# Optimization experiments

Measured on AMD Instinct MI355X. Metric: run time of the kernel, lower is better.

Reference implementation:

```python
import jax, jax.numpy as jnp
import numpy as np

# Dimensions: B graphs of NPG nodes each (equal sizes -> padding == reshape, exact)
B, NPG, DIN, H, E, DOUT, K_ORDER = 8, 4096, 128, 4, 262144, 128, 4
BETA = 0.5
N = B * NPG


def setup_inputs() -> dict:
    key = jax.random.key(0)
    k = jax.random.split(key, 12)
    s = 1.0 / np.sqrt(DIN)
    so = 1.0 / np.sqrt(H * DIN)
    x = jax.random.normal(k[0], (N, DIN), jnp.float32)
    Wq_w = jax.random.normal(k[1], (H * DIN, DIN), jnp.float32) * s
    Wq_b = jax.random.normal(k[2], (H * DIN,), jnp.float32) * 0.01
    Wk_w = jax.random.normal(k[3], (H * DIN, DIN), jnp.float32) * s
    Wk_b = jax.random.normal(k[4], (H * DIN,), jnp.float32) * 0.01
    Wo_w = jax.random.normal(k[5], (DOUT, H * DIN), jnp.float32) * so
    Wo_b = jax.random.normal(k[6], (DOUT,), jnp.float32) * 0.01
    # edges constrained within graphs (faithful to per-graph data)
    g = jax.random.randint(k[7], (E,), 0, B)
    row = g * NPG + jax.random.randint(k[8], (E,), 0, NPG)
    col = g * NPG + jax.random.randint(k[9], (E,), 0, NPG)
    edge_index = jnp.stack([row, col]).astype(jnp.int32)
    n_nodes = jnp.full((B,), NPG, jnp.int32)
    return {"x": x, "Wq_w": Wq_w, "Wq_b": Wq_b, "Wk_w": Wk_w, "Wk_b": Wk_b,
            "Wo_w": Wo_w, "Wo_b": Wo_b, "edge_index": edge_index, "n_nodes": n_nodes}


def _gcn(x, row, col):
    # x: [N,H,D]; symmetric-normalized message passing via segment sums
    deg = jax.ops.segment_sum(jnp.ones(row.shape[0], x.dtype), row, num_segments=N)
    safe = jnp.where(deg > 0, deg, 1.0)
    dis = jnp.where(deg > 0, safe ** -0.5, 0.0)
    w = (dis[row] * dis[col])[:, None, None]
    return jax.ops.segment_sum(x[col] * w, row, num_segments=N)


def _attn(qs, ks, v, n_f):
    # linear attention: out_i = (q_i . sum_j k_j v_j^T + sum_j v_j) / (q_i . sum_j k_j + n)
    q4 = qs.reshape(B, NPG, H, DIN)
    k4 = ks.reshape(B, NPG, H, DIN)
    v4 = v.reshape(B, NPG, H, DIN)
    kv = jnp.einsum('bnhd,bnhe->bhde', k4, v4)          # [B,H,D,D]
    ksum = k4.sum(axis=1)                                # [B,H,D]
    vsum = v4.sum(axis=1)                                # [B,H,D]
    num = jnp.einsum('bnhd,bhde->bnhe', q4, kv) + vsum[:, None]
    den = jnp.einsum('bnhd,bhd->bnh', q4, ksum) + n_f[:, None, None]
    return (num / den[..., None]).reshape(N, H, DIN)


def reference(x, Wq_w, Wq_b, Wk_w, Wk_b, Wo_w, Wo_b, edge_index, n_nodes):
    row, col = edge_index[0], edge_index[1]
    q = (x @ Wq_w.T + Wq_b).reshape(N, H, DIN)
    k = (x @ Wk_w.T + Wk_b).reshape(N, H, DIN)
    qs = q / jnp.linalg.norm(q, axis=2, keepdims=True)
    ks = k / jnp.linalg.norm(k, axis=2, keepdims=True)
    n_f = n_nodes.astype(x.dtype)
    xh = jnp.broadcast_to(x[:, None, :], (N, H, DIN))    # repeat over heads
    acc = xh
    cur = xh
    for _ in range(K_ORDER):
        cur = BETA * _gcn(cur, row, col) + (1.0 - BETA) * _attn(qs, ks, cur, n_f)
        acc = acc + cur
    xo = acc.reshape(N, H * DIN)
    return (xo @ Wo_w.T + Wo_b) / H
```

## Files before the change

### kernel.cpp

```cpp
#include <hip/hip_runtime.h>
#include <hip/hip_bf16.h>
#include <stdint.h>

typedef __hip_bfloat16 bf16;

#define BATCH  8
#define NPG    4096
#define DIN    128
#define NH     4
#define NEDGE  262144
#define DOUTF  128
#define KORDER 4
#define NTOT   (BATCH*NPG)
#define HD     (NH*DIN)

typedef __attribute__((ext_vector_type(8))) short short8;
typedef __attribute__((ext_vector_type(4))) float f32x4;

static __device__ __forceinline__ float b2f(bf16 v) { return __bfloat162float(v); }
static __device__ __forceinline__ float u2f(unsigned short u) {
    union { float f; unsigned int i; } c; c.i = ((unsigned int)u) << 16; return c.f;
}
static __device__ __forceinline__ unsigned short f2u(float f) {
    bf16 hb = __float2bfloat16(f);
    return *(unsigned short*)&hb;
}

__global__ void zero_kernel(uint4* p, int n) {
    int i = blockIdx.x * 256 + threadIdx.x;
    if (i < n) p[i] = uint4{0u, 0u, 0u, 0u};
}

__global__ void cvtbf_kernel(const float* __restrict__ in, bf16* __restrict__ out, int n) {
    int i = (blockIdx.x * 256 + threadIdx.x) * 8;
    if (i < n) {
        float4 a = *(const float4*)(in + i);
        float4 b = *(const float4*)(in + i + 4);
        unsigned short u[8] = { f2u(a.x), f2u(a.y), f2u(a.z), f2u(a.w),
                                f2u(b.x), f2u(b.y), f2u(b.z), f2u(b.w) };
        *(uint4*)(out + i) = *(uint4*)u;
    }
}

__global__ __launch_bounds__(256) void proj_mfma_kernel(const bf16* __restrict__ xbf,
                                                        const bf16* __restrict__ Wbf,
                                                        const float* __restrict__ bias,
                                                        bf16* __restrict__ outp,
                                                        bf16* __restrict__ outT) {
    __shared__ __align__(16) short t1[32][520];
    int n0 = blockIdx.x * 32;
    int tid = threadIdx.x;
    int lane = tid & 63, wc = tid >> 6;
    int l15 = lane & 15, quad = lane >> 4;

    f32x4 acc[2][8];
    #pragma unroll
    for (int i = 0; i < 2; i++)
        #pragma unroll
        for (int j = 0; j < 8; j++) acc[i][j] = f32x4{0.f, 0.f, 0.f, 0.f};

    #pragma unroll
    for (int ks = 0; ks < 4; ks++) {
        int kk = ks * 32 + quad * 8;
        short8 af[2];
        #pragma unroll
        for (int ti = 0; ti < 2; ti++)
            af[ti] = *(const short8*)(xbf + (size_t)(n0 + ti * 16 + l15) * DIN + kk);
        #pragma unroll
        for (int tj = 0; tj < 8; tj++) {
            short8 bfr = *(const short8*)(Wbf + (size_t)(wc * 128 + tj * 16 + l15) * DIN + kk);
            acc[0][tj] = __builtin_amdgcn_mfma_f32_16x16x32_bf16(af[0], bfr, acc[0][tj], 0, 0, 0);
            acc[1][tj] = __builtin_amdgcn_mfma_f32_16x16x32_bf16(af[1], bfr, acc[1][tj], 0, 0, 0);
        }
    }

    float bias_v[8];
    #pragma unroll
    for (int tj = 0; tj < 8; tj++) bias_v[tj] = bias[wc * 128 + tj * 16 + l15];

    #pragma unroll
    for (int ti = 0; ti < 2; ti++) {
        #pragma unroll
        for (int r = 0; r < 4; r++) {
            float s = 0.f;
            #pragma unroll
            for (int tj = 0; tj < 8; tj++) {
                float v = acc[ti][tj][r] + bias_v[tj];
                acc[ti][tj][r] = v;
                s += v * v;
            }
            s += __shfl_xor(s, 1); s += __shfl_xor(s, 2);
            s += __shfl_xor(s, 4); s += __shfl_xor(s, 8);
            float rs = rsqrtf(s);
            int node = ti * 16 + quad * 4 + r;
            #pragma unroll
            for (int tj = 0; tj < 8; tj++)
                t1[node][wc * 128 + tj * 16 + l15] = (short)f2u(acc[ti][tj][r] * rs);
        }
    }
    __syncthreads();

    if (outp) {
        #pragma unroll
        for (int u = 0; u < 8; u++) {
            int unit = u * 256 + tid;
            int nl = unit >> 6, fp = (unit & 63) * 8;
            *(uint4*)(outp + (size_t)(n0 + nl) * HD + fp) = *(uint4*)&t1[nl][fp];
        }
    }
    if (outT) {
        int b = n0 >> 12, nl0 = n0 & 4095;
        #pragma unroll
        for (int u = 0; u < 8; u++) {
            int unit = u * 256 + tid;
            int f = unit >> 2, np = (unit & 3) * 8;
            unsigned short arr[8];
            #pragma unroll
            for (int j = 0; j < 8; j++) arr[j] = (unsigned short)t1[np + j][f];
            *(uint4*)(outT + ((size_t)b * HD + f) * NPG + nl0 + np) = *(uint4*)arr;
        }
    }
}

__global__ void deg_kernel(const int* __restrict__ row, int* __restrict__ deg) {
    int e = blockIdx.x * 256 + threadIdx.x;
    if (e < NEDGE) atomicAdd(&deg[row[e]], 1);
}

__global__ void dis_kernel(const int* __restrict__ deg, float* __restrict__ dis) {
    int i = blockIdx.x * 256 + threadIdx.x;
    if (i < NTOT) {
        int d = deg[i];
        dis[i] = d > 0 ? rsqrtf((float)d) : 0.f;
    }
}

__global__ __launch_bounds__(1024) void scan1_kernel(const int* __restrict__ deg,
                                                     int* __restrict__ row_ptr, int* __restrict__ bsum) {
    __shared__ int buf[1024];
    int g = blockIdx.x, t = threadIdx.x;
    int v = deg[g * 1024 + t];
    buf[t] = v;
    __syncthreads();
    for (int off = 1; off < 1024; off <<= 1) {
        int add = (t >= off) ? buf[t - off] : 0;
        __syncthreads();
        buf[t] += add;
        __syncthreads();
    }
    row_ptr[g * 1024 + t] = buf[t] - v;
    if (t == 1023) bsum[g] = buf[1023];
}

__global__ void scan2_kernel(const int* __restrict__ bsum, int* __restrict__ boff, int* __restrict__ row_ptr) {
    int run = 0;
    for (int g = 0; g < 32; g++) { boff[g] = run; run += bsum[g]; }
    row_ptr[NTOT] = run;
}

__global__ __launch_bounds__(1024) void scan3_kernel(int* __restrict__ row_ptr, const int* __restrict__ boff) {
    row_ptr[blockIdx.x * 1024 + threadIdx.x] += boff[blockIdx.x];
}

__global__ void scatter_kernel(const int* __restrict__ row, const int* __restrict__ col,
                               const int* __restrict__ row_ptr, int* __restrict__ fill,
                               const float* __restrict__ dis,
                               int* __restrict__ col_idx, float* __restrict__ wcol) {
    int e = blockIdx.x * 256 + threadIdx.x;
    if (e < NEDGE) {
        int r = row[e], c = col[e];
        int pos = row_ptr[r] + atomicAdd(&fill[r], 1);
        col_idx[pos] = c;
        wcol[pos] = dis[c];
    }
}

__global__ __launch_bounds__(256) void rowsum_kernel(const bf16* __restrict__ T, float* __restrict__ out) {
    int row = blockIdx.x * 4 + (threadIdx.x >> 6);
    int lane = threadIdx.x & 63;
    const ushort4* p = (const ushort4*)(T + (size_t)row * NPG);
    float s = 0.f;
    #pragma unroll
    for (int wv = 0; wv < 16; wv++) {
        ushort4 u = p[lane + wv * 64];
        s += u2f(u.x) + u2f(u.y) + u2f(u.z) + u2f(u.w);
    }
    for (int off = 32; off > 0; off >>= 1) s += __shfl_down(s, off);
    if (lane == 0) out[row] = s;
}

__global__ __launch_bounds__(256) void den_kernel(const bf16* __restrict__ qs, const float* __restrict__ ksum,
                                                  const int* __restrict__ n_nodes, float* __restrict__ rden) {
    int n = blockIdx.x;
    int b = n >> 12;
    int w = threadIdx.x >> 6, lane = threadIdx.x & 63;
    int base = w * DIN;
    float p = b2f(qs[(size_t)n * HD + base + lane])      * ksum[b * HD + base + lane]
            + b2f(qs[(size_t)n * HD + base + 64 + lane]) * ksum[b * HD + base + 64 + lane];
    for (int off = 32; off > 0; off >>= 1) p += __shfl_down(p, off);
    if (lane == 0) rden[n * NH + w] = 1.0f / (p + (float)n_nodes[b]);
}

__global__ __launch_bounds__(512) void init_kernel(const bf16* __restrict__ xbf, bf16* __restrict__ cur,
                                                   bf16* __restrict__ curT, bf16* __restrict__ acc) {
    int node0 = blockIdx.x * 8;
    int t = threadIdx.x;
    int d = t & 127;
    int b = node0 >> 12, nl = node0 & 4095;
    unsigned short arr[8];
    #pragma unroll
    for (int r = 0; r < 8; r++) {
        bf16 hb = xbf[(size_t)(node0 + r) * DIN + d];
        cur[(size_t)(node0 + r) * HD + t] = hb;
        acc[(size_t)(node0 + r) * HD + t] = hb;
        arr[r] = *(unsigned short*)&hb;
    }
    *(uint4*)(curT + ((size_t)b * HD + t) * NPG + nl) = *(uint4*)arr;
}

#define KVSPLIT 8
__global__ __launch_bounds__(512, 1) void kv_mfma_kernel(const bf16* __restrict__ ksT,
                                                         const bf16* __restrict__ curT,
                                                         float* __restrict__ partial) {
    __shared__ __align__(16) short kshT[128][72];
    __shared__ __align__(16) short vshT[128][72];
    int id = blockIdx.x;
    int b = id & 7;
    int u = id >> 3;
    int h = u >> 3;
    int s = u & 7;
    int bh = b * 4 + h;
    int blk = bh * KVSPLIT + s;
    int tid = threadIdx.x;
    int lane = tid & 63;
    int w = tid >> 6;
    int wr = w >> 1, wc = w & 1;
    int d0w = wr * 32, e0w = wc * 64;
    int l15 = lane & 15, quad = lane >> 4;

    f32x4 acc[2][4];
    #pragma unroll
    for (int i = 0; i < 2; i++)
        #pragma unroll
        for (int j = 0; j < 4; j++) acc[i][j] = f32x4{0.f, 0.f, 0.f, 0.f};

    const uint4* kg = (const uint4*)(ksT + ((size_t)bh * 128) * NPG);
    const uint4* vg = (const uint4*)(curT + ((size_t)bh * 128) * NPG);
    int n0 = s * (NPG / KVSPLIT);

    for (int c = 0; c < 8; c++) {
        int nb = n0 + c * 64;
        #pragma unroll
        for (int uu = 0; uu < 2; uu++) {
            int unit = uu * 512 + tid;
            int row = unit >> 3;
            int part = unit & 7;
            int gidx = row * (NPG / 8) + (nb >> 3) + part;
            uint4 kd = kg[gidx];
            uint4 vd = vg[gidx];
            *(uint4*)&kshT[row][part * 8] = kd;
            *(uint4*)&vshT[row][part * 8] = vd;
        }
        __syncthreads();
        #pragma unroll
        for (int kkstep = 0; kkstep < 2; kkstep++) {
            int kk = kkstep * 32 + quad * 8;
            short8 af[2], bfr[4];
            #pragma unroll
            for (int ti = 0; ti < 2; ti++)
                af[ti] = *(const short8*)&kshT[d0w + ti * 16 + l15][kk];
            #pragma unroll
            for (int tj = 0; tj < 4; tj++)
                bfr[tj] = *(const short8*)&vshT[e0w + tj * 16 + l15][kk];
            #pragma unroll
            for (int ti = 0; ti < 2; ti++)
                #pragma unroll
                for (int tj = 0; tj < 4; tj++)
                    acc[ti][tj] = __builtin_amdgcn_mfma_f32_16x16x32_bf16(af[ti], bfr[tj], acc[ti][tj], 0, 0, 0);
        }
        __syncthreads();
    }
    float* p = partial + (size_t)blk * (128 * 128);
    #pragma unroll
    for (int ti = 0; ti < 2; ti++)
        #pragma unroll
        for (int tj = 0; tj < 4; tj++)
            #pragma unroll
            for (int r = 0; r < 4; r++) {
                int row = d0w + ti * 16 + quad * 4 + r;
                int col = e0w + tj * 16 + l15;
                p[row * 128 + col] = acc[ti][tj][r];
            }
}

__global__ __launch_bounds__(256) void kvredB_kernel(const float* __restrict__ partial, bf16* __restrict__ kvB) {
    __shared__ __align__(16) short t[16][136];
    int blk = blockIdx.x;
    int bh = blk >> 3;
    int e0 = (blk & 7) * 16;
    int tid = threadIdx.x;
    int el = tid & 15;
    int dc = tid >> 4;
    const float* p = partial + (size_t)bh * (KVSPLIT * 16384);
    #pragma unroll
    for (int j = 0; j < 8; j++) {
        int d = dc * 8 + j;
        int idx = d * 128 + e0 + el;
        float s = 0.f;
        #pragma unroll
        for (int sl = 0; sl < KVSPLIT; sl++) s += p[sl * 16384 + idx];
        t[el][d] = (short)f2u(s);
    }
    __syncthreads();
    int e = tid >> 4, dp = (tid & 15) * 8;
    *(uint4*)((unsigned short*)kvB + (size_t)bh * 16384 + (e0 + e) * 128 + dp) = *(uint4*)&t[e][dp];
}

__global__ __launch_bounds__(512, 2) void gcn_attn_kernel(const bf16* __restrict__ qs,
                                                          const bf16* __restrict__ kvB,
                                                          const bf16* __restrict__ cur,
                                                          const int* __restrict__ row_ptr,
                                                          const int* __restrict__ col_idx,
                                                          const float* __restrict__ wcol,
                                                          const float* __restrict__ dis,
                                                          const float* __restrict__ vsum,
                                                          const float* __restrict__ rden,
                                                          bf16* __restrict__ curN,
                                                          bf16* __restrict__ curTN,
                                                          bf16* __restrict__ accb,
                                                          float* __restrict__ vsumN) {
    __shared__ __align__(16) short t1[128][136];
    int id = blockIdx.x;
    int b = id & 7;
    int u = id >> 3;
    int h = u >> 5;
    int m = u & 31;
    int bh = b * 4 + h;
    int n0 = b * NPG + m * 128;
    int tid = threadIdx.x;
    int lane = tid & 63, w = tid >> 6;
    int wr = w >> 1, wc = w & 1;
    int e0w = wc * 64;
    int l15 = lane & 15, quad = lane >> 4;

    {
        int nl = tid >> 2;
        int sub = tid & 3;
        int n = n0 + nl;
        int start = row_ptr[n], end = row_ptr[n + 1];
        float g[32];
        #pragma unroll
        for (int i = 0; i < 32; i++) g[i] = 0.f;
        const bf16* gbase = cur + (size_t)h * DIN + sub * 32;
        int c0 = 0; float w0 = 0.f;
        if (start < end) { c0 = col_idx[start]; w0 = wcol[start]; }
        uint4 vb[4];
        {
            const uint4* p = (const uint4*)(gbase + (size_t)c0 * HD);
            vb[0] = p[0]; vb[1] = p[1]; vb[2] = p[2]; vb[3] = p[3];
        }
        for (int j = start; j < end; j++) {
            int c1 = c0; float w1 = 0.f;
            if (j + 1 < end) { c1 = col_idx[j + 1]; w1 = wcol[j + 1]; }
            const uint4* p = (const uint4*)(gbase + (size_t)c1 * HD);
            uint4 vn0 = p[0], vn1 = p[1], vn2 = p[2], vn3 = p[3];
            #pragma unroll
            for (int q = 0; q < 4; q++) {
                unsigned short* sv = (unsigned short*)&vb[q];
                #pragma unroll
                for (int k = 0; k < 8; k++) g[q * 8 + k] += w0 * u2f(sv[k]);
            }
            vb[0] = vn0; vb[1] = vn1; vb[2] = vn2; vb[3] = vn3;
            w0 = w1;
        }
        float dn = dis[n];
        int sw = (nl >> 3) & 7;
        #pragma unroll
        for (int q = 0; q < 4; q++) {
            unsigned short arr[8];
            #pragma unroll
            for (int k = 0; k < 8; k++) arr[k] = f2u(g[q * 8 + k] * dn);
            int fb = (sub * 4 + q) ^ sw;
            *(uint4*)&t1[nl][fb * 8] = *(uint4*)arr;
        }
    }

    f32x4 acc[2][4];
    #pragma unroll
    for (int i = 0; i < 2; i++)
        #pragma unroll
        for (int j = 0; j < 4; j++) acc[i][j] = f32x4{0.f, 0.f, 0.f, 0.f};

    const bf16* Aq = qs + (size_t)n0 * HD + h * DIN;
    const unsigned short* Bk = (const unsigned short*)kvB + (size_t)bh * 16384;
    #pragma unroll
    for (int ks = 0; ks < 4; ks++) {
        int kk = ks * 32 + quad * 8;
        short8 af[2], bfr[4];
        #pragma unroll
        for (int ti = 0; ti < 2; ti++)
            af[ti] = *(const short8*)(Aq + (size_t)(wr * 32 + ti * 16 + l15) * HD + kk);
        #pragma unroll
        for (int tj = 0; tj < 4; tj++)
            bfr[tj] = *(const short8*)(Bk + (e0w + tj * 16 + l15) * 128 + kk);
        #pragma unroll
        for (int ti = 0; ti < 2; ti++)
            #pragma unroll
            for (int tj = 0; tj < 4; tj++)
                acc[ti][tj] = __builtin_amdgcn_mfma_f32_16x16x32_bf16(af[ti], bfr[tj], acc[ti][tj], 0, 0, 0);
    }
    __syncthreads();

    #pragma unroll
    for (int tj = 0; tj < 4; tj++) {
        int el = e0w + tj * 16 + l15;
        float vs = vsum[b * HD + h * DIN + el];
        float cs = 0.f;
        #pragma unroll
        for (int ti = 0; ti < 2; ti++) {
            int nlb = wr * 32 + ti * 16 + quad * 4;
            #pragma unroll
            for (int r = 0; r < 4; r++) {
                int nl = nlb + r;
                int sw = (nl >> 3) & 7;
                int pc = (((el >> 3) ^ sw) * 8) | (el & 7);
                float attnv = (acc[ti][tj][r] + vs) * rden[(size_t)(n0 + nl) * NH + h];
                float g = u2f((unsigned short)t1[nl][pc]);
                float val = 0.5f * g + 0.5f * attnv;
                t1[nl][pc] = (short)f2u(val);
                cs += val;
            }
        }
        cs += __shfl_xor(cs, 16);
        cs += __shfl_xor(cs, 32);
        if (quad == 0) atomicAdd(&vsumN[b * HD + h * DIN + el], cs);
    }
    __syncthreads();

    {
        bf16* dstn = curN + (size_t)n0 * HD + h * DIN;
        bf16* dsta = accb + (size_t)n0 * HD + h * DIN;
        #pragma unroll
        for (int uu = 0; uu < 4; uu++) {
            int unit = uu * 512 + tid;
            int nl = unit >> 4, fb = unit & 15;
            int sw = (nl >> 3) & 7;
            uint4 v = *(uint4*)&t1[nl][(fb ^ sw) * 8];
            *(uint4*)(dstn + (size_t)nl * HD + fb * 8) = v;
            unsigned short* sv = (unsigned short*)&v;
            unsigned short* ap = (unsigned short*)(dsta + (size_t)nl * HD + fb * 8);
            uint4 a = *(uint4*)ap;
            unsigned short* av = (unsigned short*)&a;
            unsigned short res[8];
            #pragma unroll
            for (int j = 0; j < 8; j++) res[j] = f2u(u2f(av[j]) + u2f(sv[j]));
            *(uint4*)ap = *(uint4*)res;
        }
    }
    {
        bf16* dstT = curTN + ((size_t)b * HD + h * DIN) * NPG + m * 128;
        #pragma unroll
        for (int uu = 0; uu < 4; uu++) {
            int unit = uu * 512 + tid;
            int fl = unit >> 4, np = (unit & 15) * 8;
            unsigned short arr[8];
            #pragma unroll
            for (int j = 0; j < 8; j++) {
                int row = np + j;
                int sw = (row >> 3) & 7;
                int pc = (((fl >> 3) ^ sw) * 8) | (fl & 7);
                arr[j] = (unsigned short)t1[row][pc];
            }
            *(uint4*)(dstT + (size_t)fl * NPG + np) = *(uint4*)arr;
        }
    }
}

__global__ __launch_bounds__(512) void out_mfma_kernel(const bf16* __restrict__ accb,
                                                       const bf16* __restrict__ Wobf,
                                                       const float* __restrict__ Wo_b,
                                                       float* __restrict__ out) {
    int n0 = blockIdx.x * 128;
    int tid = threadIdx.x;
    int lane = tid & 63, w = tid >> 6;
    int wr = w >> 1, wc = w & 1;
    int l15 = lane & 15, quad = lane >> 4;

    f32x4 acc[2][4];
    #pragma unroll
    for (int i = 0; i < 2; i++)
        #pragma unroll
        for (int j = 0; j < 4; j++) acc[i][j] = f32x4{0.f, 0.f, 0.f, 0.f};

    for (int ks = 0; ks < 16; ks++) {
        int kk = ks * 32 + quad * 8;
        short8 af[2], bfr[4];
        #pragma unroll
        for (int ti = 0; ti < 2; ti++)
            af[ti] = *(const short8*)(accb + (size_t)(n0 + wr * 32 + ti * 16 + l15) * HD + kk);
        #pragma unroll
        for (int tj = 0; tj < 4; tj++)
            bfr[tj] = *(const short8*)(Wobf + (size_t)(wc * 64 + tj * 16 + l15) * HD + kk);
        #pragma unroll
        for (int ti = 0; ti < 2; ti++)
            #pragma unroll
            for (int tj = 0; tj < 4; tj++)
                acc[ti][tj] = __builtin_amdgcn_mfma_f32_16x16x32_bf16(af[ti], bfr[tj], acc[ti][tj], 0, 0, 0);
    }

    #pragma unroll
    for (int tj = 0; tj < 4; tj++) {
        int col = wc * 64 + tj * 16 + l15;
        float bv = Wo_b[col];
        #pragma unroll
        for (int ti = 0; ti < 2; ti++) {
            int rowb = wr * 32 + ti * 16 + quad * 4;
            #pragma unroll
            for (int r = 0; r < 4; r++)
                out[(size_t)(n0 + rowb + r) * DOUTF + col] = (acc[ti][tj][r] + bv) * 0.25f;
        }
    }
}

extern "C" void kernel_launch(void* const* d_in, const int* in_sizes, int n_in,
                              void* d_out, int out_size, void* d_ws, size_t ws_size,
                              hipStream_t stream) {
    const float* x     = (const float*)d_in[0];
    const float* Wq_w  = (const float*)d_in[1];
    const float* Wq_b  = (const float*)d_in[2];
    const float* Wk_w  = (const float*)d_in[3];
    const float* Wk_b  = (const float*)d_in[4];
    const float* Wo_w  = (const float*)d_in[5];
    const float* Wo_b  = (const float*)d_in[6];
    const int*   edge  = (const int*)d_in[7];
    const int*   n_nod = (const int*)d_in[8];
    float* out = (float*)d_out;
    const int* erow = edge;
    const int* ecol = edge + NEDGE;

    char* w = (char*)d_ws;
    auto alloc = [&](size_t bytes) -> char* {
        char* p = w;
        w += (bytes + 255) & ~(size_t)255;
        return p;
    };
    bf16*  qs      = (bf16*) alloc((size_t)NTOT * HD * 2);
    bf16*  ksT     = (bf16*) alloc((size_t)NTOT * HD * 2);
    bf16*  curA    = (bf16*) alloc((size_t)NTOT * HD * 2);
    bf16*  curB    = (bf16*) alloc((size_t)NTOT * HD * 2);
    bf16*  curTA   = (bf16*) alloc((size_t)NTOT * HD * 2);
    bf16*  curTB   = (bf16*) alloc((size_t)NTOT * HD * 2);
    bf16*  accb    = (bf16*) alloc((size_t)NTOT * HD * 2);
    float* partial = (float*)alloc((size_t)32 * KVSPLIT * 16384 * 4);
    bf16*  kvB     = (bf16*) alloc((size_t)32 * 16384 * 2);
    bf16*  Wobf    = (bf16*) alloc(DOUTF * HD * 2);
    int*   degfill = (int*)  alloc(2 * NTOT * 4);
    float* dis     = (float*)alloc(NTOT * 4);
    int*   row_ptr = (int*)  alloc((NTOT + 1) * 4);
    int*   col_idx = (int*)  alloc(NEDGE * 4);
    float* wcol    = (float*)alloc(NEDGE * 4);
    float* ksum    = (float*)alloc(BATCH * HD * 4);
    float* vsumA   = (float*)alloc(BATCH * HD * 4);
    float* vsumB   = (float*)alloc(BATCH * HD * 4);
    float* rden    = (float*)alloc((size_t)NTOT * NH * 4);
    int*   bsum    = (int*)  alloc(32 * 4);
    int*   boff    = (int*)  alloc(32 * 4);
    int* deg  = degfill;
    int* fill = degfill + NTOT;
    bf16* xbf  = (bf16*)partial;
    bf16* Wqbf = (bf16*)((char*)partial + (8 << 20));
    bf16* Wkbf = Wqbf + (size_t)HD * DIN;

    zero_kernel<<<64, 256, 0, stream>>>((uint4*)degfill, 2 * NTOT / 4);

    cvtbf_kernel<<<NTOT * DIN / 8 / 256, 256, 0, stream>>>(x, xbf, NTOT * DIN);
    cvtbf_kernel<<<HD * DIN / 8 / 256, 256, 0, stream>>>(Wq_w, Wqbf, HD * DIN);
    cvtbf_kernel<<<HD * DIN / 8 / 256, 256, 0, stream>>>(Wk_w, Wkbf, HD * DIN);
    cvtbf_kernel<<<DOUTF * HD / 8 / 256, 256, 0, stream>>>(Wo_w, Wobf, DOUTF * HD);

    proj_mfma_kernel<<<NTOT / 32, 256, 0, stream>>>(xbf, Wqbf, Wq_b, qs, (bf16*)nullptr);
    proj_mfma_kernel<<<NTOT / 32, 256, 0, stream>>>(xbf, Wkbf, Wk_b, (bf16*)nullptr, ksT);

    deg_kernel<<<NEDGE / 256, 256, 0, stream>>>(erow, deg);
    dis_kernel<<<NTOT / 256, 256, 0, stream>>>(deg, dis);
    scan1_kernel<<<32, 1024, 0, stream>>>(deg, row_ptr, bsum);
    scan2_kernel<<<1, 1, 0, stream>>>(bsum, boff, row_ptr);
    scan3_kernel<<<32, 1024, 0, stream>>>(row_ptr, boff);
    scatter_kernel<<<NEDGE / 256, 256, 0, stream>>>(erow, ecol, row_ptr, fill, dis, col_idx, wcol);

    rowsum_kernel<<<BATCH * HD / 4, 256, 0, stream>>>(ksT, ksum);
    den_kernel<<<NTOT, 256, 0, stream>>>(qs, ksum, n_nod, rden);

    init_kernel<<<NTOT / 8, 512, 0, stream>>>(xbf, curA, curTA, accb);
    rowsum_kernel<<<BATCH * HD / 4, 256, 0, stream>>>(curTA, vsumA);

    bf16* c = curA;  bf16* cT = curTA;
    bf16* cn = curB; bf16* cnT = curTB;
    float* vs = vsumA;
    float* vsN = vsumB;
    for (int it = 0; it < KORDER; it++) {
        kv_mfma_kernel<<<32 * KVSPLIT, 512, 0, stream>>>(ksT, cT, partial);
        kvredB_kernel<<<256, 256, 0, stream>>>(partial, kvB);
        zero_kernel<<<4, 256, 0, stream>>>((uint4*)vsN, BATCH * HD / 4);
        gcn_attn_kernel<<<32 * 32, 512, 0, stream>>>(qs, kvB, c, row_ptr, col_idx, wcol, dis,
                                                     vs, rden, cn, cnT, accb, vsN);
        bf16* t;
        t = c; c = cn; cn = t;
        t = cT; cT = cnT; cnT = t;
        float* tf = vs; vs = vsN; vsN = tf;
    }

    out_mfma_kernel<<<NTOT / 128, 512, 0, stream>>>(accb, Wobf, Wo_b, out);

    (void)in_sizes; (void)n_in; (void)out_size; (void)ws_size;
}
```

Baseline: 622.4 us.

## Pack CSR col/weight pairs, stage edges in LDS, double-buffer gathers in GCN

Column indices and edge weights are packed into one uint2 array, so the scatter writes once and the reader loads once. Each gcn_attn block now stages its 128 nodes' edge list into shared memory, with a global-memory fallback when the count exceeds a cap. The neighbour gather loop is unrolled by two, keeping two rows of loads in flight to hide gather latency. The cost is extra LDS, a block barrier and more registers, which may lower occupancy at 512 threads with 2 blocks per CU.

```diff
diff --git a/kernel.cpp b/kernel.cpp
--- a/kernel.cpp
+++ b/kernel.cpp
@@ -165,13 +165,12 @@
 __global__ void scatter_kernel(const int* __restrict__ row, const int* __restrict__ col,
                                const int* __restrict__ row_ptr, int* __restrict__ fill,
                                const float* __restrict__ dis,
-                               int* __restrict__ col_idx, float* __restrict__ wcol) {
+                               uint2* __restrict__ ecw) {
     int e = blockIdx.x * 256 + threadIdx.x;
     if (e < NEDGE) {
         int r = row[e], c = col[e];
         int pos = row_ptr[r] + atomicAdd(&fill[r], 1);
-        col_idx[pos] = c;
-        wcol[pos] = dis[c];
+        ecw[pos] = uint2{(unsigned)c, __float_as_uint(dis[c])};
     }
 }
 
@@ -316,12 +315,18 @@
     *(uint4*)((unsigned short*)kvB + (size_t)bh * 16384 + (e0 + e) * 128 + dp) = *(uint4*)&t[e][dp];
 }
 
+static __device__ __forceinline__ void acc8(float* g, uint4 v, float w) {
+    unsigned short* sv = (unsigned short*)&v;
+    #pragma unroll
+    for (int k = 0; k < 8; k++) g[k] += w * u2f(sv[k]);
+}
+
+#define EMAX 1536
 __global__ __launch_bounds__(512, 2) void gcn_attn_kernel(const bf16* __restrict__ qs,
                                                           const bf16* __restrict__ kvB,
                                                           const bf16* __restrict__ cur,
                                                           const int* __restrict__ row_ptr,
-                                                          const int* __restrict__ col_idx,
-                                                          const float* __restrict__ wcol,
+                                                          const uint2* __restrict__ ecw,
                                                           const float* __restrict__ dis,
                                                           const float* __restrict__ vsum,
                                                           const float* __restrict__ rden,
@@ -330,6 +335,7 @@
                                                           bf16* __restrict__ accb,
                                                           float* __restrict__ vsumN) {
     __shared__ __align__(16) short t1[128][136];
+    __shared__ __align__(8) uint2 est[EMAX];
     int id = blockIdx.x;
     int b = id & 7;
     int u = id >> 3;
@@ -343,36 +349,63 @@
     int e0w = wc * 64;
     int l15 = lane & 15, quad = lane >> 4;
 
+    int ebase = row_ptr[n0];
+    int ecnt = row_ptr[n0 + 128] - ebase;
+    int scnt = ecnt < EMAX ? ecnt : EMAX;
+    for (int i = tid; i < scnt; i += 512) est[i] = ecw[ebase + i];
+    __syncthreads();
+
     {
         int nl = tid >> 2;
         int sub = tid & 3;
         int n = n0 + nl;
-        int start = row_ptr[n], end = row_ptr[n + 1];
+        int start = row_ptr[n] - ebase;
+        int end   = row_ptr[n + 1] - ebase;
+        int lend  = end < scnt ? end : scnt;
         float g[32];
         #pragma unroll
         for (int i = 0; i < 32; i++) g[i] = 0.f;
         const bf16* gbase = cur + (size_t)h * DIN + sub * 32;
-        int c0 = 0; float w0 = 0.f;
-        if (start < end) { c0 = col_idx[start]; w0 = wcol[start]; }
-        uint4 vb[4];
+
+        int cA = 0, cB = 0; float wA = 0.f, wB = 0.f;
+        if (start < lend)     { uint2 p = est[start];     cA = (int)p.x; wA = __uint_as_float(p.y); }
+        if (start + 1 < lend) { uint2 p = est[start + 1]; cB = (int)p.x; wB = __uint_as_float(p.y); }
+        uint4 vA0, vA1, vA2, vA3, vB0, vB1, vB2, vB3;
         {
-            const uint4* p = (const uint4*)(gbase + (size_t)c0 * HD);
-            vb[0] = p[0]; vb[1] = p[1]; vb[2] = p[2]; vb[3] = p[3];
-        }
-        for (int j = start; j < end; j++) {
-            int c1 = c0; float w1 = 0.f;
-            if (j + 1 < end) { c1 = col_idx[j + 1]; w1 = wcol[j + 1]; }
-            const uint4* p = (const uint4*)(gbase + (size_t)c1 * HD);
-            uint4 vn0 = p[0], vn1 = p[1], vn2 = p[2], vn3 = p[3];
-            #pragma unroll
-            for (int q = 0; q < 4; q++) {
-                unsigned short* sv = (unsigned short*)&vb[q];
-                #pragma unroll
-                for (int k = 0; k < 8; k++) g[q * 8 + k] += w0 * u2f(sv[k]);
+            const uint4* p = (const uint4*)(gbase + (size_t)cA * HD);
+            vA0 = p[0]; vA1 = p[1]; vA2 = p[2]; vA3 = p[3];
+        }
+        {
+            const uint4* p = (const uint4*)(gbase + (size_t)cB * HD);
+            vB0 = p[0]; vB1 = p[1]; vB2 = p[2]; vB3 = p[3];
+        }
+        for (int j = start; j < lend; j += 2) {
+            int cC = 0, cD = 0; float wC = 0.f, wD = 0.f;
+            if (j + 2 < lend) { uint2 p = est[j + 2]; cC = (int)p.x; wC = __uint_as_float(p.y); }
+            if (j + 3 < lend) { uint2 p = est[j + 3]; cD = (int)p.x; wD = __uint_as_float(p.y); }
+            acc8(g +  0, vA0, wA); acc8(g +  8, vA1, wA);
+            acc8(g + 16, vA2, wA); acc8(g + 24, vA3, wA);
+            {
+                const uint4* p = (const uint4*)(gbase + (size_t)cC * HD);
+                vA0 = p[0]; vA1 = p[1]; vA2 = p[2]; vA3 = p[3];
             }
-            vb[0] = vn0; vb[1] = vn1; vb[2] = vn2; vb[3] = vn3;
-            w0 = w1;
-        }
+            acc8(g +  0, vB0, wB); acc8(g +  8, vB1, wB);
+            acc8(g + 16, vB2, wB); acc8(g + 24, vB3, wB);
+            {
+                const uint4* p = (const uint4*)(gbase + (size_t)cD * HD);
+                vB0 = p[0]; vB1 = p[1]; vB2 = p[2]; vB3 = p[3];
+            }
+            wA = wC; wB = wD;
+        }
+        int fstart = start > lend ? start : lend;
+        for (int j = fstart; j < end; j++) {
+            uint2 pe = ecw[ebase + j];
+            int c = (int)pe.x; float ww = __uint_as_float(pe.y);
+            const uint4* p = (const uint4*)(gbase + (size_t)c * HD);
+            acc8(g +  0, p[0], ww); acc8(g +  8, p[1], ww);
+            acc8(g + 16, p[2], ww); acc8(g + 24, p[3], ww);
+        }
+
         float dn = dis[n];
         int sw = (nl >> 3) & 7;
         #pragma unroll
@@ -557,8 +590,7 @@
     int*   degfill = (int*)  alloc(2 * NTOT * 4);
     float* dis     = (float*)alloc(NTOT * 4);
     int*   row_ptr = (int*)  alloc((NTOT + 1) * 4);
-    int*   col_idx = (int*)  alloc(NEDGE * 4);
-    float* wcol    = (float*)alloc(NEDGE * 4);
+    uint2* ecw     = (uint2*)alloc((size_t)NEDGE * 8);
     float* ksum    = (float*)alloc(BATCH * HD * 4);
     float* vsumA   = (float*)alloc(BATCH * HD * 4);
     float* vsumB   = (float*)alloc(BATCH * HD * 4);
@@ -586,7 +618,7 @@
     scan1_kernel<<<32, 1024, 0, stream>>>(deg, row_ptr, bsum);
     scan2_kernel<<<1, 1, 0, stream>>>(bsum, boff, row_ptr);
     scan3_kernel<<<32, 1024, 0, stream>>>(row_ptr, boff);
-    scatter_kernel<<<NEDGE / 256, 256, 0, stream>>>(erow, ecol, row_ptr, fill, dis, col_idx, wcol);
+    scatter_kernel<<<NEDGE / 256, 256, 0, stream>>>(erow, ecol, row_ptr, fill, dis, ecw);
 
     rowsum_kernel<<<BATCH * HD / 4, 256, 0, stream>>>(ksT, ksum);
     den_kernel<<<NTOT, 256, 0, stream>>>(qs, ksum, n_nod, rden);
@@ -602,7 +634,7 @@
         kv_mfma_kernel<<<32 * KVSPLIT, 512, 0, stream>>>(ksT, cT, partial);
         kvredB_kernel<<<256, 256, 0, stream>>>(partial, kvB);
         zero_kernel<<<4, 256, 0, stream>>>((uint4*)vsN, BATCH * HD / 4);
-        gcn_attn_kernel<<<32 * 32, 512, 0, stream>>>(qs, kvB, c, row_ptr, col_idx, wcol, dis,
+        gcn_attn_kernel<<<32 * 32, 512, 0, stream>>>(qs, kvB, c, row_ptr, ecw, dis,
                                                      vs, rden, cn, cnT, accb, vsN);
         bf16* t;
         t = c; c = cn; cn = t;
```

Result: faster. 608.8 us (-2.2%).
